# Performance work log

Measured on AMD Instinct MI355X. Metric: run time of the kernel, lower is better.

The kernel has to match this reference:

```python
import jax, jax.numpy as jnp
import numpy as np

N, E, F_IN, H, D, HID, G = 50000, 800000, 64, 4, 32, 128, 1024
NEG_SLOPE = 0.2


def setup_inputs():
    key = jax.random.key(0)
    ks = jax.random.split(key, 32)
    inp = {
        "x": jax.random.normal(ks[0], (N, F_IN), dtype=jnp.float32),
        "edge_index": jax.random.randint(ks[1], (2, E), 0, N, dtype=jnp.int64),
        "batch": jnp.sort(jax.random.randint(ks[2], (N,), 0, G, dtype=jnp.int64)),
    }
    dims = [F_IN, HID, HID]
    i = 3
    for l, din in enumerate(dims):
        s = 1.0 / np.sqrt(din)
        inp[f"Wl{l}"] = jax.random.normal(ks[i], (din, H * D), dtype=jnp.float32) * s; i += 1
        inp[f"bl{l}"] = jnp.zeros((H * D,), dtype=jnp.float32)
        inp[f"Wr{l}"] = jax.random.normal(ks[i], (din, H * D), dtype=jnp.float32) * s; i += 1
        inp[f"br{l}"] = jnp.zeros((H * D,), dtype=jnp.float32)
        inp[f"att{l}"] = jax.random.normal(ks[i], (H, D), dtype=jnp.float32) * (1.0 / np.sqrt(D)); i += 1
        inp[f"b{l}"] = jnp.zeros((H * D,), dtype=jnp.float32)
    inp["Wh"] = jax.random.normal(ks[i], (HID, 1), dtype=jnp.float32) * (1.0 / np.sqrt(HID))
    inp["bh"] = jnp.zeros((1,), dtype=jnp.float32)
    return inp


def gatv2_layer(x, src, dst, Wl, bl, Wr, br, att, b):
    # GATv2Conv (eval mode, no dropout): e_ij = att . leaky_relu(Wl x_j + Wr x_i)
    xl = (x @ Wl + bl).reshape(-1, H, D)   # source transform
    xr = (x @ Wr + br).reshape(-1, H, D)   # target transform
    m = xl[src] + xr[dst]                  # [E,H,D]
    e = jnp.where(m >= 0, m, NEG_SLOPE * m)
    score = jnp.einsum("ehd,hd->eh", e, att)          # [E,H]
    smax = jax.ops.segment_max(score, dst, num_segments=N)  # [N,H]
    expv = jnp.exp(score - smax[dst])
    denom = jax.ops.segment_sum(expv, dst, num_segments=N)
    alpha = expv / denom[dst]                          # softmax over in-edges of dst
    agg = jax.ops.segment_sum(alpha[:, :, None] * xl[src], dst, num_segments=N)
    return agg.reshape(-1, H * D) + b


def reference(x, edge_index, batch, Wl0, bl0, Wr0, br0, att0, b0,
              Wl1, bl1, Wr1, br1, att1, b1,
              Wl2, bl2, Wr2, br2, att2, b2, Wh, bh):
    src, dst = edge_index[0], edge_index[1]
    params = [(Wl0, bl0, Wr0, br0, att0, b0),
              (Wl1, bl1, Wr1, br1, att1, b1),
              (Wl2, bl2, Wr2, br2, att2, b2)]
    h = x
    for p in params:
        h = gatv2_layer(h, src, dst, *p)
        h = jax.nn.elu(h)  # dropout inactive in eval
    # global mean pool over graphs
    sums = jax.ops.segment_sum(h, batch, num_segments=G)
    cnt = jax.ops.segment_sum(jnp.ones((h.shape[0],), h.dtype), batch, num_segments=G)
    pooled = sums / jnp.maximum(cnt, 1.0)[:, None]
    return pooled @ Wh + bh
```

## Files before the change

### kernel.cpp

```cpp
#include <hip/hip_runtime.h>
#include <math.h>

#define N_NODES 50000
#define N_EDGES 800000
#define HD 128
#define GG 1024
#define NEG_SLOPE 0.2f
#define SCAN_B 1024
#define NB ((N_NODES + SCAN_B - 1) / SCAN_B)
#define NXCONV (N_NODES * 64)

typedef __attribute__((ext_vector_type(8))) short bf16x8;
typedef __attribute__((ext_vector_type(4))) float f32x4;

__device__ __forceinline__ unsigned short f2bf(float v) {
    unsigned u = __float_as_uint(v);
    u += 0x7fff + ((u >> 16) & 1);
    return (unsigned short)(u >> 16);
}
__device__ __forceinline__ float bf2f(unsigned short s) {
    return __uint_as_float((unsigned)s << 16);
}

__global__ void convert_all(const float* __restrict__ x,
                            unsigned short* __restrict__ Xh, unsigned short* __restrict__ Xl,
                            const float* __restrict__ W0l, const float* __restrict__ W0r,
                            const float* __restrict__ W1l, const float* __restrict__ W1r,
                            const float* __restrict__ W2l, const float* __restrict__ W2r,
                            unsigned short* __restrict__ Wth, unsigned short* __restrict__ Wtl,
                            int* __restrict__ deg)
{
    const int i = blockIdx.x * 256 + threadIdx.x;
    if (i < N_NODES) deg[i] = 0;
    if (i < NXCONV) {
        const float v = x[i];
        const unsigned short hi = f2bf(v);
        Xh[i] = hi;
        Xl[i] = f2bf(v - bf2f(hi));
        return;
    }
    const int t = i - NXCONV;
    const float* Wl; const float* Wr;
    int c, k, o;
    if (t < 16384) {
        c = t >> 6; k = t & 63; o = t;
        Wl = W0l; Wr = W0r;
    } else if (t < 49152) {
        const int b = t - 16384; c = b >> 7; k = b & 127; o = 32768 + b;
        Wl = W1l; Wr = W1r;
    } else if (t < 81920) {
        const int b = t - 49152; c = b >> 7; k = b & 127; o = 65536 + b;
        Wl = W2l; Wr = W2r;
    } else return;
    const float v = (c < 128) ? Wl[(size_t)k * 128 + c] : Wr[(size_t)k * 128 + (c - 128)];
    const unsigned short hi = f2bf(v);
    Wth[o] = hi;
    Wtl[o] = f2bf(v - bf2f(hi));
}

__global__ void prep_graph(const int* __restrict__ dst, int* __restrict__ deg,
                           const int* __restrict__ batch, int* __restrict__ gptr)
{
    const int e = blockIdx.x * 256 + threadIdx.x;
    if (e < N_EDGES) atomicAdd(&deg[dst[e]], 1);
    if (e > N_NODES) return;
    if (e == 0) {
        for (int g = 0; g <= batch[0]; g++) gptr[g] = 0;
    } else if (e == N_NODES) {
        for (int g = batch[N_NODES - 1] + 1; g <= GG; g++) gptr[g] = N_NODES;
    } else {
        const int b0 = batch[e - 1], b1 = batch[e];
        for (int g = b0 + 1; g <= b1; g++) gptr[g] = e;
    }
}

template<int K>
__launch_bounds__(256, 3)
__global__ void gemm_lds(const unsigned short* __restrict__ Xh, const unsigned short* __restrict__ Xl,
                         const unsigned short* __restrict__ Wth, const unsigned short* __restrict__ Wtl,
                         const float* __restrict__ bl, const float* __restrict__ br,
                         float* __restrict__ Cl, float* __restrict__ Cr, int n)
{
    constexpr int NCH = K / 32;
    constexpr int STR = K + 8;
    __shared__ unsigned short AsH[64 * STR], AsL[64 * STR];
    const int tid  = threadIdx.x;
    const int wave = tid >> 6;
    const int lane = tid & 63;
    const int quad = lane >> 4;
    const int l15  = lane & 15;
    const int cg   = blockIdx.x & 1;
    const int rt   = blockIdx.x >> 1;
    const int row0 = rt * 64;
    const int colid = cg * 4 + wave;
    const int cb32  = colid * 32;

    bf16x8 Bh[NCH][2], Bo[NCH][2];
    #pragma unroll
    for (int ch = 0; ch < NCH; ch++)
        #pragma unroll
        for (int nt = 0; nt < 2; nt++) {
            const size_t wo = (size_t)(cb32 + nt * 16 + l15) * K + ch * 32 + quad * 8;
            Bh[ch][nt] = *(const bf16x8*)(Wth + wo);
            Bo[ch][nt] = *(const bf16x8*)(Wtl + wo);
        }

    {
        constexpr int THR = K / 8;
        constexpr int RPP = 256 / THR;
        const int sr = tid / THR, seg = tid % THR;
        #pragma unroll
        for (int ps = 0; ps < 64 / RPP; ps++) {
            const int r = ps * RPP + sr;
            int gr = row0 + r;
            gr = (gr < n) ? gr : (n - 1);
            const size_t go = (size_t)gr * K + seg * 8;
            *(uint4*)&AsH[r * STR + seg * 8] = *(const uint4*)(Xh + go);
            *(uint4*)&AsL[r * STR + seg * 8] = *(const uint4*)(Xl + go);
        }
    }
    __syncthreads();

    f32x4 acc[4][2];
    #pragma unroll
    for (int mt = 0; mt < 4; mt++) {
        acc[mt][0] = (f32x4){0.f, 0.f, 0.f, 0.f};
        acc[mt][1] = (f32x4){0.f, 0.f, 0.f, 0.f};
    }
    #pragma unroll
    for (int ch = 0; ch < NCH; ch++) {
        bf16x8 ah[4], al[4];
        #pragma unroll
        for (int mt = 0; mt < 4; mt++) {
            ah[mt] = *(const bf16x8*)&AsH[(mt * 16 + l15) * STR + ch * 32 + quad * 8];
            al[mt] = *(const bf16x8*)&AsL[(mt * 16 + l15) * STR + ch * 32 + quad * 8];
        }
        #pragma unroll
        for (int nt = 0; nt < 2; nt++)
            #pragma unroll
            for (int mt = 0; mt < 4; mt++) {
                acc[mt][nt] = __builtin_amdgcn_mfma_f32_16x16x32_bf16(ah[mt], Bh[ch][nt], acc[mt][nt], 0, 0, 0);
                acc[mt][nt] = __builtin_amdgcn_mfma_f32_16x16x32_bf16(ah[mt], Bo[ch][nt], acc[mt][nt], 0, 0, 0);
                acc[mt][nt] = __builtin_amdgcn_mfma_f32_16x16x32_bf16(al[mt], Bh[ch][nt], acc[mt][nt], 0, 0, 0);
            }
    }

    const int cb = cb32 & 127;
    const float* bias = (colid < 4) ? bl : br;
    float* C = (colid < 4) ? Cl : Cr;
    const float bv0 = bias[cb + l15];
    const float bv1 = bias[cb + 16 + l15];
    #pragma unroll
    for (int nt = 0; nt < 2; nt++) {
        const float bv = nt ? bv1 : bv0;
        #pragma unroll
        for (int mt = 0; mt < 4; mt++)
            #pragma unroll
            for (int r = 0; r < 4; r++) {
                const int row = row0 + mt * 16 + quad * 4 + r;
                if (row < n)
                    C[(size_t)row * 128 + cb + nt * 16 + l15] = acc[mt][nt][r] + bv;
            }
    }
}

__launch_bounds__(SCAN_B)
__global__ void scan_block(const int* __restrict__ deg, int* __restrict__ rowptr,
                           int* __restrict__ btot)
{
    __shared__ int s[SCAN_B];
    const int tid = threadIdx.x;
    const int i = blockIdx.x * SCAN_B + tid;
    int v = (i < N_NODES) ? deg[i] : 0;
    s[tid] = v;
    __syncthreads();
    for (int off = 1; off < SCAN_B; off <<= 1) {
        int t = (tid >= off) ? s[tid - off] : 0;
        __syncthreads();
        s[tid] += t;
        __syncthreads();
    }
    if (i < N_NODES) rowptr[i] = s[tid] - v;
    if (tid == SCAN_B - 1) btot[blockIdx.x] = s[SCAN_B - 1];
}

__launch_bounds__(256)
__global__ void scan_add(const int* __restrict__ btot, int* __restrict__ rowptr,
                         int* __restrict__ cursor)
{
    __shared__ int sb[NB + 1];
    const int tid = threadIdx.x;
    if (tid < 64) {
        const int v = (tid < NB) ? btot[tid] : 0;
        int incl = v;
        #pragma unroll
        for (int off = 1; off < 64; off <<= 1) {
            const int t = __shfl_up(incl, off);
            if (tid >= off) incl += t;
        }
        if (tid < NB) sb[tid] = incl - v;
        if (tid == NB - 1) sb[NB] = incl;
    }
    __syncthreads();
    const int i = blockIdx.x * 256 + tid;
    if (i < N_NODES) {
        const int r = rowptr[i] + sb[i >> 10];
        rowptr[i] = r;
        cursor[i] = r;
    }
    if (i == N_NODES) rowptr[N_NODES] = sb[NB];
}

__global__ void scatter_csr(const int* __restrict__ src, const int* __restrict__ dst,
                            int* __restrict__ cursor, int* __restrict__ csr_src)
{
    int e = blockIdx.x * 256 + threadIdx.x;
    if (e >= N_EDGES) return;
    int pos = atomicAdd(&cursor[dst[e]], 1);
    csr_src[pos] = src[e];
}

template<int LAST>
__launch_bounds__(256)
__global__ void node_attn(const float* __restrict__ xl, const float* __restrict__ xr,
                          const int* __restrict__ rowptr, const int* __restrict__ csr_src,
                          const float* __restrict__ att, const float* __restrict__ bvec,
                          unsigned short* __restrict__ Hh, unsigned short* __restrict__ Hl,
                          const float* __restrict__ Wh, float* __restrict__ pernode)
{
    const int node = (blockIdx.x * 256 + threadIdx.x) >> 6;
    const int lane = threadIdx.x & 63;
    if (node >= N_NODES) return;
    const int grp = lane >> 4;
    const int li  = lane & 15;

    const size_t nb = (size_t)node * HD + li * 8;
    const float4 xr0 = *(const float4*)(xr + nb);
    const float4 xr1 = *(const float4*)(xr + nb + 4);
    const float4 aw0 = *(const float4*)(att + li * 8);
    const float4 aw1 = *(const float4*)(att + li * 8 + 4);
    const int beg = rowptr[node];
    const int end = rowptr[node + 1];

    float m = -1e30f, l = 0.f;
    float4 a0 = make_float4(0.f, 0.f, 0.f, 0.f);
    float4 a1 = make_float4(0.f, 0.f, 0.f, 0.f);

    int e0 = beg + grp;
    int s0 = (e0 < end) ? csr_src[e0] : 0;
    float4 v0 = *(const float4*)(xl + (size_t)s0 * HD + li * 8);
    float4 v1 = *(const float4*)(xl + (size_t)s0 * HD + li * 8 + 4);

    for (int base = beg; base < end; base += 4) {
        const bool valid = (base + grp) < end;
        float4 n0 = v0, n1 = v1;
        if (base + 4 < end) {
            const int e2 = base + 4 + grp;
            const int s2 = (e2 < end) ? csr_src[e2] : 0;
            n0 = *(const float4*)(xl + (size_t)s2 * HD + li * 8);
            n1 = *(const float4*)(xl + (size_t)s2 * HD + li * 8 + 4);
        }
        float t, pa, pb;
        t = v0.x + xr0.x; t = fmaxf(t, NEG_SLOPE * t); pa = t * aw0.x;
        t = v0.y + xr0.y; t = fmaxf(t, NEG_SLOPE * t); pb = t * aw0.y;
        t = v0.z + xr0.z; t = fmaxf(t, NEG_SLOPE * t); pa = fmaf(t, aw0.z, pa);
        t = v0.w + xr0.w; t = fmaxf(t, NEG_SLOPE * t); pb = fmaf(t, aw0.w, pb);
        t = v1.x + xr1.x; t = fmaxf(t, NEG_SLOPE * t); pa = fmaf(t, aw1.x, pa);
        t = v1.y + xr1.y; t = fmaxf(t, NEG_SLOPE * t); pb = fmaf(t, aw1.y, pb);
        t = v1.z + xr1.z; t = fmaxf(t, NEG_SLOPE * t); pa = fmaf(t, aw1.z, pa);
        t = v1.w + xr1.w; t = fmaxf(t, NEG_SLOPE * t); pb = fmaf(t, aw1.w, pb);
        float p = pa + pb;
        p += __shfl_xor(p, 1);
        p += __shfl_xor(p, 2);

        const float mn = valid ? fmaxf(m, p) : m;
        const float w  = valid ? __expf(p - mn) : 0.f;
        const float sc = __expf(m - mn);
        l = fmaf(l, sc, w);
        a0.x = fmaf(a0.x, sc, w * v0.x);
        a0.y = fmaf(a0.y, sc, w * v0.y);
        a0.z = fmaf(a0.z, sc, w * v0.z);
        a0.w = fmaf(a0.w, sc, w * v0.w);
        a1.x = fmaf(a1.x, sc, w * v1.x);
        a1.y = fmaf(a1.y, sc, w * v1.y);
        a1.z = fmaf(a1.z, sc, w * v1.z);
        a1.w = fmaf(a1.w, sc, w * v1.w);
        m = mn;
        v0 = n0; v1 = n1;
    }

    #pragma unroll
    for (int off = 16; off < 64; off <<= 1) {
        const float mo = __shfl_xor(m, off);
        const float lo = __shfl_xor(l, off);
        float4 b0, b1;
        b0.x = __shfl_xor(a0.x, off); b0.y = __shfl_xor(a0.y, off);
        b0.z = __shfl_xor(a0.z, off); b0.w = __shfl_xor(a0.w, off);
        b1.x = __shfl_xor(a1.x, off); b1.y = __shfl_xor(a1.y, off);
        b1.z = __shfl_xor(a1.z, off); b1.w = __shfl_xor(a1.w, off);
        const float mm = fmaxf(m, mo);
        const float e1 = __expf(m - mm);
        const float e2 = __expf(mo - mm);
        l = l * e1 + lo * e2;
        a0.x = a0.x * e1 + b0.x * e2;
        a0.y = a0.y * e1 + b0.y * e2;
        a0.z = a0.z * e1 + b0.z * e2;
        a0.w = a0.w * e1 + b0.w * e2;
        a1.x = a1.x * e1 + b1.x * e2;
        a1.y = a1.y * e1 + b1.y * e2;
        a1.z = a1.z * e1 + b1.z * e2;
        a1.w = a1.w * e1 + b1.w * e2;
        m = mm;
    }

    if (grp == 0) {
        const float inv = (l > 0.f) ? 1.f / l : 0.f;
        const float4 bb0 = *(const float4*)(bvec + li * 8);
        const float4 bb1 = *(const float4*)(bvec + li * 8 + 4);
        float o[8];
        o[0] = fmaf(a0.x, inv, bb0.x);
        o[1] = fmaf(a0.y, inv, bb0.y);
        o[2] = fmaf(a0.z, inv, bb0.z);
        o[3] = fmaf(a0.w, inv, bb0.w);
        o[4] = fmaf(a1.x, inv, bb1.x);
        o[5] = fmaf(a1.y, inv, bb1.y);
        o[6] = fmaf(a1.z, inv, bb1.z);
        o[7] = fmaf(a1.w, inv, bb1.w);
        #pragma unroll
        for (int j = 0; j < 8; j++)
            o[j] = (o[j] > 0.f) ? o[j] : expm1f(o[j]);
        if (LAST) {
            const float4 w0 = *(const float4*)(Wh + li * 8);
            const float4 w1 = *(const float4*)(Wh + li * 8 + 4);
            float da = o[0] * w0.x + o[2] * w0.z;
            float db = o[1] * w0.y + o[3] * w0.w;
            da = fmaf(o[4], w1.x, da); db = fmaf(o[5], w1.y, db);
            da = fmaf(o[6], w1.z, da); db = fmaf(o[7], w1.w, db);
            float d = da + db;
            d += __shfl_xor(d, 1);
            d += __shfl_xor(d, 2);
            d += __shfl_xor(d, 4);
            d += __shfl_xor(d, 8);
            if (li == 0) pernode[node] = d;
        } else {
            bf16x8 hv, lv;
            #pragma unroll
            for (int j = 0; j < 8; j++) {
                unsigned short h = f2bf(o[j]);
                hv[j] = (short)h;
                lv[j] = (short)f2bf(o[j] - bf2f(h));
            }
            *(bf16x8*)(Hh + nb) = hv;
            *(bf16x8*)(Hl + nb) = lv;
        }
    }
}

__launch_bounds__(256)
__global__ void finish_head(const float* __restrict__ pernode, const int* __restrict__ gptr,
                            const float* __restrict__ bh, float* __restrict__ out)
{
    const int g = (blockIdx.x * 256 + threadIdx.x) >> 6;
    const int lane = threadIdx.x & 63;
    if (g >= GG) return;
    const int b0 = gptr[g], b1 = gptr[g + 1];
    float s = 0.f;
    for (int i = b0 + lane; i < b1; i += 64) s += pernode[i];
    s += __shfl_xor(s, 1);
    s += __shfl_xor(s, 2);
    s += __shfl_xor(s, 4);
    s += __shfl_xor(s, 8);
    s += __shfl_xor(s, 16);
    s += __shfl_xor(s, 32);
    if (lane == 0) out[g] = s / fmaxf((float)(b1 - b0), 1.f) + bh[0];
}

extern "C" void kernel_launch(void* const* d_in, const int* in_sizes, int n_in,
                              void* d_out, int out_size, void* d_ws, size_t ws_size,
                              hipStream_t stream)
{
    const float* x     = (const float*)d_in[0];
    const int*   edge  = (const int*)d_in[1];
    const int*   batch = (const int*)d_in[2];
    const int*   src   = edge;
    const int*   dst   = edge + N_EDGES;
    const float* Wh    = (const float*)d_in[21];
    const float* bh    = (const float*)d_in[22];
    float* out = (float*)d_out;

    const size_t N128 = (size_t)N_NODES * HD;
    float* buf_xl = (float*)d_ws;
    float* buf_xr = buf_xl + N128;
    unsigned short* Xh  = (unsigned short*)(buf_xr + N128);
    unsigned short* Xl_ = Xh + N128;
    unsigned short* Wth = Xl_ + N128;
    unsigned short* Wtl = Wth + 3 * 256 * 128;
    int* deg       = (int*)(Wtl + 3 * 256 * 128);
    float* pernode = (float*)(deg + N_NODES);
    int* rowptr  = (int*)(pernode + N_NODES);
    int* cursor  = rowptr + N_NODES + 1;
    int* csr_src = cursor + N_NODES;
    int* btot    = csr_src + N_EDGES;
    int* gptr    = btot + NB;

    convert_all<<<(NXCONV + 81920 + 255) / 256, 256, 0, stream>>>(
        x, Xh, Xl_,
        (const float*)d_in[3], (const float*)d_in[5],
        (const float*)d_in[9], (const float*)d_in[11],
        (const float*)d_in[15], (const float*)d_in[17],
        Wth, Wtl, deg);
    prep_graph<<<(N_EDGES + 255) / 256, 256, 0, stream>>>(dst, deg, batch, gptr);
    scan_block<<<NB, SCAN_B, 0, stream>>>(deg, rowptr, btot);
    scan_add<<<(N_NODES + 256) / 256, 256, 0, stream>>>(btot, rowptr, cursor);
    scatter_csr<<<(N_EDGES + 255) / 256, 256, 0, stream>>>(src, dst, cursor, csr_src);

    const int gemm_grid = ((N_NODES + 63) / 64) * 2;
    const int attn_grid = (N_NODES + 3) / 4;

    for (int l = 0; l < 3; l++) {
        const float* bl  = (const float*)d_in[4 + 6 * l];
        const float* br  = (const float*)d_in[6 + 6 * l];
        const float* att = (const float*)d_in[7 + 6 * l];
        const float* bb  = (const float*)d_in[8 + 6 * l];

        if (l == 0)
            gemm_lds<64><<<gemm_grid, 256, 0, stream>>>(Xh, Xl_, Wth, Wtl,
                                                        bl, br, buf_xl, buf_xr, N_NODES);
        else
            gemm_lds<128><<<gemm_grid, 256, 0, stream>>>(Xh, Xl_,
                                                         Wth + l * 256 * 128, Wtl + l * 256 * 128,
                                                         bl, br, buf_xl, buf_xr, N_NODES);
        if (l < 2)
            node_attn<0><<<attn_grid, 256, 0, stream>>>(buf_xl, buf_xr, rowptr, csr_src,
                                                        att, bb, Xh, Xl_,
                                                        nullptr, nullptr);
        else
            node_attn<1><<<attn_grid, 256, 0, stream>>>(buf_xl, buf_xr, rowptr, csr_src,
                                                        att, bb, nullptr, nullptr,
                                                        Wh, pernode);
    }

    finish_head<<<GG / 4, 256, 0, stream>>>(pernode, gptr, bh, out);
}
```

Baseline: 478.5 us.

## Merge prep kernels, single-block scan, persistent GEMM grid, packed f32x2 attention math

Fuses conversion and graph-prep into one launch, with deg zeroed by a memset. The two-kernel scan is replaced by a single 1024-thread block that scans 49 elements per thread. The GEMM becomes a persistent grid-stride loop over row tiles with a fixed grid of 512, with B fragments loaded once per block and the occupancy hint dropped. The attention inner loop uses 2-wide float vectors, aiming for packed FP32 instructions. Together these cut launch count and per-block weight reloads, at the cost of a serial single-block scan and possibly lower GEMM occupancy.

```diff
diff --git a/kernel.cpp b/kernel.cpp
--- a/kernel.cpp
+++ b/kernel.cpp
@@ -6,12 +6,12 @@
 #define HD 128
 #define GG 1024
 #define NEG_SLOPE 0.2f
-#define SCAN_B 1024
-#define NB ((N_NODES + SCAN_B - 1) / SCAN_B)
 #define NXCONV (N_NODES * 64)
+#define NWCONV 81920
 
 typedef __attribute__((ext_vector_type(8))) short bf16x8;
 typedef __attribute__((ext_vector_type(4))) float f32x4;
+typedef __attribute__((ext_vector_type(2))) float f32x2;
 
 __device__ __forceinline__ unsigned short f2bf(float v) {
     unsigned u = __float_as_uint(v);
@@ -22,16 +22,16 @@
     return __uint_as_float((unsigned)s << 16);
 }
 
-__global__ void convert_all(const float* __restrict__ x,
-                            unsigned short* __restrict__ Xh, unsigned short* __restrict__ Xl,
-                            const float* __restrict__ W0l, const float* __restrict__ W0r,
-                            const float* __restrict__ W1l, const float* __restrict__ W1r,
-                            const float* __restrict__ W2l, const float* __restrict__ W2r,
-                            unsigned short* __restrict__ Wth, unsigned short* __restrict__ Wtl,
-                            int* __restrict__ deg)
+__global__ void convert_prep(const float* __restrict__ x,
+                             unsigned short* __restrict__ Xh, unsigned short* __restrict__ Xl,
+                             const float* __restrict__ W0l, const float* __restrict__ W0r,
+                             const float* __restrict__ W1l, const float* __restrict__ W1r,
+                             const float* __restrict__ W2l, const float* __restrict__ W2r,
+                             unsigned short* __restrict__ Wth, unsigned short* __restrict__ Wtl,
+                             const int* __restrict__ dst, int* __restrict__ deg,
+                             const int* __restrict__ batch, int* __restrict__ gptr)
 {
     const int i = blockIdx.x * 256 + threadIdx.x;
-    if (i < N_NODES) deg[i] = 0;
     if (i < NXCONV) {
         const float v = x[i];
         const unsigned short hi = f2bf(v);
@@ -39,29 +39,27 @@
         Xl[i] = f2bf(v - bf2f(hi));
         return;
     }
-    const int t = i - NXCONV;
-    const float* Wl; const float* Wr;
-    int c, k, o;
-    if (t < 16384) {
-        c = t >> 6; k = t & 63; o = t;
-        Wl = W0l; Wr = W0r;
-    } else if (t < 49152) {
-        const int b = t - 16384; c = b >> 7; k = b & 127; o = 32768 + b;
-        Wl = W1l; Wr = W1r;
-    } else if (t < 81920) {
-        const int b = t - 49152; c = b >> 7; k = b & 127; o = 65536 + b;
-        Wl = W2l; Wr = W2r;
-    } else return;
-    const float v = (c < 128) ? Wl[(size_t)k * 128 + c] : Wr[(size_t)k * 128 + (c - 128)];
-    const unsigned short hi = f2bf(v);
-    Wth[o] = hi;
-    Wtl[o] = f2bf(v - bf2f(hi));
-}
-
-__global__ void prep_graph(const int* __restrict__ dst, int* __restrict__ deg,
-                           const int* __restrict__ batch, int* __restrict__ gptr)
-{
-    const int e = blockIdx.x * 256 + threadIdx.x;
+    if (i < NXCONV + NWCONV) {
+        const int t = i - NXCONV;
+        const float* Wl; const float* Wr;
+        int c, k, o;
+        if (t < 16384) {
+            c = t >> 6; k = t & 63; o = t;
+            Wl = W0l; Wr = W0r;
+        } else if (t < 49152) {
+            const int b = t - 16384; c = b >> 7; k = b & 127; o = 32768 + b;
+            Wl = W1l; Wr = W1r;
+        } else {
+            const int b = t - 49152; c = b >> 7; k = b & 127; o = 65536 + b;
+            Wl = W2l; Wr = W2r;
+        }
+        const float v = (c < 128) ? Wl[(size_t)k * 128 + c] : Wr[(size_t)k * 128 + (c - 128)];
+        const unsigned short hi = f2bf(v);
+        Wth[o] = hi;
+        Wtl[o] = f2bf(v - bf2f(hi));
+        return;
+    }
+    const int e = i - NXCONV - NWCONV;
     if (e < N_EDGES) atomicAdd(&deg[dst[e]], 1);
     if (e > N_NODES) return;
     if (e == 0) {
@@ -74,8 +72,52 @@
     }
 }
 
+#define SPT 49
+__launch_bounds__(1024)
+__global__ void scan_all(const int* __restrict__ deg, int* __restrict__ rowptr,
+                         int* __restrict__ cursor)
+{
+    __shared__ int ps[1024];
+    const int tid = threadIdx.x;
+    const int base = tid * SPT;
+    int s = 0;
+    #pragma unroll
+    for (int j = 0; j < SPT; j++) {
+        const int idx = base + j;
+        s += (idx < N_NODES) ? deg[idx] : 0;
+    }
+    ps[tid] = s;
+    __syncthreads();
+    for (int off = 1; off < 1024; off <<= 1) {
+        const int t = (tid >= off) ? ps[tid - off] : 0;
+        __syncthreads();
+        ps[tid] += t;
+        __syncthreads();
+    }
+    int run = ps[tid] - s;
+    #pragma unroll
+    for (int j = 0; j < SPT; j++) {
+        const int idx = base + j;
+        if (idx < N_NODES) {
+            rowptr[idx] = run;
+            cursor[idx] = run;
+            run += deg[idx];
+        }
+    }
+    if (tid == 1023) rowptr[N_NODES] = ps[1023];
+}
+
+__global__ void scatter_csr(const int* __restrict__ src, const int* __restrict__ dst,
+                            int* __restrict__ cursor, int* __restrict__ csr_src)
+{
+    int e = blockIdx.x * 256 + threadIdx.x;
+    if (e >= N_EDGES) return;
+    int pos = atomicAdd(&cursor[dst[e]], 1);
+    csr_src[pos] = src[e];
+}
+
 template<int K>
-__launch_bounds__(256, 3)
+__launch_bounds__(256)
 __global__ void gemm_lds(const unsigned short* __restrict__ Xh, const unsigned short* __restrict__ Xl,
                          const unsigned short* __restrict__ Wth, const unsigned short* __restrict__ Wtl,
                          const float* __restrict__ bl, const float* __restrict__ br,
@@ -83,6 +125,7 @@
 {
     constexpr int NCH = K / 32;
     constexpr int STR = K + 8;
+    constexpr int RT  = (N_NODES + 63) / 64;
     __shared__ unsigned short AsH[64 * STR], AsL[64 * STR];
     const int tid  = threadIdx.x;
     const int wave = tid >> 6;
@@ -90,8 +133,8 @@
     const int quad = lane >> 4;
     const int l15  = lane & 15;
     const int cg   = blockIdx.x & 1;
-    const int rt   = blockIdx.x >> 1;
-    const int row0 = rt * 64;
+    const int rs   = blockIdx.x >> 1;
+    const int NS   = gridDim.x >> 1;
     const int colid = cg * 4 + wave;
     const int cb32  = colid * 32;
 
@@ -104,120 +147,69 @@
             Bh[ch][nt] = *(const bf16x8*)(Wth + wo);
             Bo[ch][nt] = *(const bf16x8*)(Wtl + wo);
         }
-
-    {
-        constexpr int THR = K / 8;
-        constexpr int RPP = 256 / THR;
-        const int sr = tid / THR, seg = tid % THR;
-        #pragma unroll
-        for (int ps = 0; ps < 64 / RPP; ps++) {
-            const int r = ps * RPP + sr;
-            int gr = row0 + r;
-            gr = (gr < n) ? gr : (n - 1);
-            const size_t go = (size_t)gr * K + seg * 8;
-            *(uint4*)&AsH[r * STR + seg * 8] = *(const uint4*)(Xh + go);
-            *(uint4*)&AsL[r * STR + seg * 8] = *(const uint4*)(Xl + go);
-        }
-    }
-    __syncthreads();
-
-    f32x4 acc[4][2];
-    #pragma unroll
-    for (int mt = 0; mt < 4; mt++) {
-        acc[mt][0] = (f32x4){0.f, 0.f, 0.f, 0.f};
-        acc[mt][1] = (f32x4){0.f, 0.f, 0.f, 0.f};
-    }
-    #pragma unroll
-    for (int ch = 0; ch < NCH; ch++) {
-        bf16x8 ah[4], al[4];
-        #pragma unroll
-        for (int mt = 0; mt < 4; mt++) {
-            ah[mt] = *(const bf16x8*)&AsH[(mt * 16 + l15) * STR + ch * 32 + quad * 8];
-            al[mt] = *(const bf16x8*)&AsL[(mt * 16 + l15) * STR + ch * 32 + quad * 8];
-        }
-        #pragma unroll
-        for (int nt = 0; nt < 2; nt++)
-            #pragma unroll
-            for (int mt = 0; mt < 4; mt++) {
-                acc[mt][nt] = __builtin_amdgcn_mfma_f32_16x16x32_bf16(ah[mt], Bh[ch][nt], acc[mt][nt], 0, 0, 0);
-                acc[mt][nt] = __builtin_amdgcn_mfma_f32_16x16x32_bf16(ah[mt], Bo[ch][nt], acc[mt][nt], 0, 0, 0);
-                acc[mt][nt] = __builtin_amdgcn_mfma_f32_16x16x32_bf16(al[mt], Bh[ch][nt], acc[mt][nt], 0, 0, 0);
-            }
-    }
 
     const int cb = cb32 & 127;
     const float* bias = (colid < 4) ? bl : br;
     float* C = (colid < 4) ? Cl : Cr;
     const float bv0 = bias[cb + l15];
     const float bv1 = bias[cb + 16 + l15];
-    #pragma unroll
-    for (int nt = 0; nt < 2; nt++) {
-        const float bv = nt ? bv1 : bv0;
-        #pragma unroll
-        for (int mt = 0; mt < 4; mt++)
+
+    for (int rt = rs; rt < RT; rt += NS) {
+        const int row0 = rt * 64;
+        {
+            constexpr int THR = K / 8;
+            constexpr int RPP = 256 / THR;
+            const int sr = tid / THR, seg = tid % THR;
             #pragma unroll
-            for (int r = 0; r < 4; r++) {
-                const int row = row0 + mt * 16 + quad * 4 + r;
-                if (row < n)
-                    C[(size_t)row * 128 + cb + nt * 16 + l15] = acc[mt][nt][r] + bv;
+            for (int ps = 0; ps < 64 / RPP; ps++) {
+                const int r = ps * RPP + sr;
+                int gr = row0 + r;
+                gr = (gr < n) ? gr : (n - 1);
+                const size_t go = (size_t)gr * K + seg * 8;
+                *(uint4*)&AsH[r * STR + seg * 8] = *(const uint4*)(Xh + go);
+                *(uint4*)&AsL[r * STR + seg * 8] = *(const uint4*)(Xl + go);
             }
-    }
-}
-
-__launch_bounds__(SCAN_B)
-__global__ void scan_block(const int* __restrict__ deg, int* __restrict__ rowptr,
-                           int* __restrict__ btot)
-{
-    __shared__ int s[SCAN_B];
-    const int tid = threadIdx.x;
-    const int i = blockIdx.x * SCAN_B + tid;
-    int v = (i < N_NODES) ? deg[i] : 0;
-    s[tid] = v;
-    __syncthreads();
-    for (int off = 1; off < SCAN_B; off <<= 1) {
-        int t = (tid >= off) ? s[tid - off] : 0;
+        }
         __syncthreads();
-        s[tid] += t;
+
+        f32x4 acc[4][2];
+        #pragma unroll
+        for (int mt = 0; mt < 4; mt++) {
+            acc[mt][0] = (f32x4){0.f, 0.f, 0.f, 0.f};
+            acc[mt][1] = (f32x4){0.f, 0.f, 0.f, 0.f};
+        }
+        #pragma unroll
+        for (int ch = 0; ch < NCH; ch++) {
+            bf16x8 ah[4], al[4];
+            #pragma unroll
+            for (int mt = 0; mt < 4; mt++) {
+                ah[mt] = *(const bf16x8*)&AsH[(mt * 16 + l15) * STR + ch * 32 + quad * 8];
+                al[mt] = *(const bf16x8*)&AsL[(mt * 16 + l15) * STR + ch * 32 + quad * 8];
+            }
+            #pragma unroll
+            for (int nt = 0; nt < 2; nt++)
+                #pragma unroll
+                for (int mt = 0; mt < 4; mt++) {
+                    acc[mt][nt] = __builtin_amdgcn_mfma_f32_16x16x32_bf16(ah[mt], Bh[ch][nt], acc[mt][nt], 0, 0, 0);
+                    acc[mt][nt] = __builtin_amdgcn_mfma_f32_16x16x32_bf16(ah[mt], Bo[ch][nt], acc[mt][nt], 0, 0, 0);
+                    acc[mt][nt] = __builtin_amdgcn_mfma_f32_16x16x32_bf16(al[mt], Bh[ch][nt], acc[mt][nt], 0, 0, 0);
+                }
+        }
+
+        #pragma unroll
+        for (int nt = 0; nt < 2; nt++) {
+            const float bv = nt ? bv1 : bv0;
+            #pragma unroll
+            for (int mt = 0; mt < 4; mt++)
+                #pragma unroll
+                for (int r = 0; r < 4; r++) {
+                    const int row = row0 + mt * 16 + quad * 4 + r;
+                    if (row < n)
+                        C[(size_t)row * 128 + cb + nt * 16 + l15] = acc[mt][nt][r] + bv;
+                }
+        }
         __syncthreads();
     }
-    if (i < N_NODES) rowptr[i] = s[tid] - v;
-    if (tid == SCAN_B - 1) btot[blockIdx.x] = s[SCAN_B - 1];
-}
-
-__launch_bounds__(256)
-__global__ void scan_add(const int* __restrict__ btot, int* __restrict__ rowptr,
-                         int* __restrict__ cursor)
-{
-    __shared__ int sb[NB + 1];
-    const int tid = threadIdx.x;
-    if (tid < 64) {
-        const int v = (tid < NB) ? btot[tid] : 0;
-        int incl = v;
-        #pragma unroll
-        for (int off = 1; off < 64; off <<= 1) {
-            const int t = __shfl_up(incl, off);
-            if (tid >= off) incl += t;
-        }
-        if (tid < NB) sb[tid] = incl - v;
-        if (tid == NB - 1) sb[NB] = incl;
-    }
-    __syncthreads();
-    const int i = blockIdx.x * 256 + tid;
-    if (i < N_NODES) {
-        const int r = rowptr[i] + sb[i >> 10];
-        rowptr[i] = r;
-        cursor[i] = r;
-    }
-    if (i == N_NODES) rowptr[N_NODES] = sb[NB];
-}
-
-__global__ void scatter_csr(const int* __restrict__ src, const int* __restrict__ dst,
-                            int* __restrict__ cursor, int* __restrict__ csr_src)
-{
-    int e = blockIdx.x * 256 + threadIdx.x;
-    if (e >= N_EDGES) return;
-    int pos = atomicAdd(&cursor[dst[e]], 1);
-    csr_src[pos] = src[e];
 }
 
 template<int LAST>
@@ -235,41 +227,61 @@
     const int li  = lane & 15;
 
     const size_t nb = (size_t)node * HD + li * 8;
-    const float4 xr0 = *(const float4*)(xr + nb);
-    const float4 xr1 = *(const float4*)(xr + nb + 4);
-    const float4 aw0 = *(const float4*)(att + li * 8);
-    const float4 aw1 = *(const float4*)(att + li * 8 + 4);
+    f32x2 xrp[4], awp[4];
+    {
+        const float4 a = *(const float4*)(xr + nb);
+        const float4 b = *(const float4*)(xr + nb + 4);
+        xrp[0] = (f32x2){a.x, a.y}; xrp[1] = (f32x2){a.z, a.w};
+        xrp[2] = (f32x2){b.x, b.y}; xrp[3] = (f32x2){b.z, b.w};
+        const float4 c = *(const float4*)(att + li * 8);
+        const float4 d = *(const float4*)(att + li * 8 + 4);
+        awp[0] = (f32x2){c.x, c.y}; awp[1] = (f32x2){c.z, c.w};
+        awp[2] = (f32x2){d.x, d.y}; awp[3] = (f32x2){d.z, d.w};
+    }
+    const f32x2 nsl = (f32x2){NEG_SLOPE, NEG_SLOPE};
     const int beg = rowptr[node];
     const int end = rowptr[node + 1];
 
     float m = -1e30f, l = 0.f;
-    float4 a0 = make_float4(0.f, 0.f, 0.f, 0.f);
-    float4 a1 = make_float4(0.f, 0.f, 0.f, 0.f);
-
-    int e0 = beg + grp;
-    int s0 = (e0 < end) ? csr_src[e0] : 0;
-    float4 v0 = *(const float4*)(xl + (size_t)s0 * HD + li * 8);
-    float4 v1 = *(const float4*)(xl + (size_t)s0 * HD + li * 8 + 4);
+    f32x2 accp[4];
+    #pragma unroll
+    for (int j = 0; j < 4; j++) accp[j] = (f32x2){0.f, 0.f};
+
+    f32x2 vp[4];
+    {
+        const int e0 = beg + grp;
+        const int s0 = (e0 < end) ? csr_src[e0] : 0;
+        const float4 a = *(const float4*)(xl + (size_t)s0 * HD + li * 8);
+        const float4 b = *(const float4*)(xl + (size_t)s0 * HD + li * 8 + 4);
+        vp[0] = (f32x2){a.x, a.y}; vp[1] = (f32x2){a.z, a.w};
+        vp[2] = (f32x2){b.x, b.y}; vp[3] = (f32x2){b.z, b.w};
+    }
 
     for (int base = beg; base < end; base += 4) {
         const bool valid = (base + grp) < end;
-        float4 n0 = v0, n1 = v1;
+        f32x2 np[4];
+        #pragma unroll
+        for (int j = 0; j < 4; j++) np[j] = vp[j];
         if (base + 4 < end) {
             const int e2 = base + 4 + grp;
             const int s2 = (e2 < end) ? csr_src[e2] : 0;
-            n0 = *(const float4*)(xl + (size_t)s2 * HD + li * 8);
-            n1 = *(const float4*)(xl + (size_t)s2 * HD + li * 8 + 4);
-        }
-        float t, pa, pb;
-        t = v0.x + xr0.x; t = fmaxf(t, NEG_SLOPE * t); pa = t * aw0.x;
-        t = v0.y + xr0.y; t = fmaxf(t, NEG_SLOPE * t); pb = t * aw0.y;
-        t = v0.z + xr0.z; t = fmaxf(t, NEG_SLOPE * t); pa = fmaf(t, aw0.z, pa);
-        t = v0.w + xr0.w; t = fmaxf(t, NEG_SLOPE * t); pb = fmaf(t, aw0.w, pb);
-        t = v1.x + xr1.x; t = fmaxf(t, NEG_SLOPE * t); pa = fmaf(t, aw1.x, pa);
-        t = v1.y + xr1.y; t = fmaxf(t, NEG_SLOPE * t); pb = fmaf(t, aw1.y, pb);
-        t = v1.z + xr1.z; t = fmaxf(t, NEG_SLOPE * t); pa = fmaf(t, aw1.z, pa);
-        t = v1.w + xr1.w; t = fmaxf(t, NEG_SLOPE * t); pb = fmaf(t, aw1.w, pb);
-        float p = pa + pb;
+            const float4 a = *(const float4*)(xl + (size_t)s2 * HD + li * 8);
+            const float4 b = *(const float4*)(xl + (size_t)s2 * HD + li * 8 + 4);
+            np[0] = (f32x2){a.x, a.y}; np[1] = (f32x2){a.z, a.w};
+            np[2] = (f32x2){b.x, b.y}; np[3] = (f32x2){b.z, b.w};
+        }
+        f32x2 pd0 = (f32x2){0.f, 0.f}, pd1 = (f32x2){0.f, 0.f};
+        #pragma unroll
+        for (int j = 0; j < 4; j++) {
+            f32x2 t = vp[j] + xrp[j];
+            const f32x2 u = t * nsl;
+            t[0] = fmaxf(t[0], u[0]);
+            t[1] = fmaxf(t[1], u[1]);
+            if (j & 1) pd1 = t * awp[j] + pd1;
+            else       pd0 = t * awp[j] + pd0;
+        }
+        const f32x2 pds = pd0 + pd1;
+        float p = pds[0] + pds[1];
         p += __shfl_xor(p, 1);
         p += __shfl_xor(p, 2);
 
@@ -277,39 +289,35 @@
         const float w  = valid ? __expf(p - mn) : 0.f;
         const float sc = __expf(m - mn);
         l = fmaf(l, sc, w);
-        a0.x = fmaf(a0.x, sc, w * v0.x);
-        a0.y = fmaf(a0.y, sc, w * v0.y);
-        a0.z = fmaf(a0.z, sc, w * v0.z);
-        a0.w = fmaf(a0.w, sc, w * v0.w);
-        a1.x = fmaf(a1.x, sc, w * v1.x);
-        a1.y = fmaf(a1.y, sc, w * v1.y);
-        a1.z = fmaf(a1.z, sc, w * v1.z);
-        a1.w = fmaf(a1.w, sc, w * v1.w);
+        const f32x2 w2  = (f32x2){w, w};
+        const f32x2 sc2 = (f32x2){sc, sc};
+        #pragma unroll
+        for (int j = 0; j < 4; j++) {
+            accp[j] = accp[j] * sc2 + w2 * vp[j];
+            vp[j] = np[j];
+        }
         m = mn;
-        v0 = n0; v1 = n1;
     }
 
     #pragma unroll
     for (int off = 16; off < 64; off <<= 1) {
         const float mo = __shfl_xor(m, off);
         const float lo = __shfl_xor(l, off);
-        float4 b0, b1;
-        b0.x = __shfl_xor(a0.x, off); b0.y = __shfl_xor(a0.y, off);
-        b0.z = __shfl_xor(a0.z, off); b0.w = __shfl_xor(a0.w, off);
-        b1.x = __shfl_xor(a1.x, off); b1.y = __shfl_xor(a1.y, off);
-        b1.z = __shfl_xor(a1.z, off); b1.w = __shfl_xor(a1.w, off);
+        f32x2 bo[4];
+        #pragma unroll
+        for (int j = 0; j < 4; j++) {
+            bo[j][0] = __shfl_xor(accp[j][0], off);
+            bo[j][1] = __shfl_xor(accp[j][1], off);
+        }
         const float mm = fmaxf(m, mo);
         const float e1 = __expf(m - mm);
         const float e2 = __expf(mo - mm);
         l = l * e1 + lo * e2;
-        a0.x = a0.x * e1 + b0.x * e2;
-        a0.y = a0.y * e1 + b0.y * e2;
-        a0.z = a0.z * e1 + b0.z * e2;
-        a0.w = a0.w * e1 + b0.w * e2;
-        a1.x = a1.x * e1 + b1.x * e2;
-        a1.y = a1.y * e1 + b1.y * e2;
-        a1.z = a1.z * e1 + b1.z * e2;
-        a1.w = a1.w * e1 + b1.w * e2;
+        const f32x2 e1p = (f32x2){e1, e1};
+        const f32x2 e2p = (f32x2){e2, e2};
+        #pragma unroll
+        for (int j = 0; j < 4; j++)
+            accp[j] = accp[j] * e1p + bo[j] * e2p;
         m = mm;
     }
 
@@ -318,14 +326,14 @@
         const float4 bb0 = *(const float4*)(bvec + li * 8);
         const float4 bb1 = *(const float4*)(bvec + li * 8 + 4);
         float o[8];
-        o[0] = fmaf(a0.x, inv, bb0.x);
-        o[1] = fmaf(a0.y, inv, bb0.y);
-        o[2] = fmaf(a0.z, inv, bb0.z);
-        o[3] = fmaf(a0.w, inv, bb0.w);
-        o[4] = fmaf(a1.x, inv, bb1.x);
-        o[5] = fmaf(a1.y, inv, bb1.y);
-        o[6] = fmaf(a1.z, inv, bb1.z);
-        o[7] = fmaf(a1.w, inv, bb1.w);
+        o[0] = fmaf(accp[0][0], inv, bb0.x);
+        o[1] = fmaf(accp[0][1], inv, bb0.y);
+        o[2] = fmaf(accp[1][0], inv, bb0.z);
+        o[3] = fmaf(accp[1][1], inv, bb0.w);
+        o[4] = fmaf(accp[2][0], inv, bb1.x);
+        o[5] = fmaf(accp[2][1], inv, bb1.y);
+        o[6] = fmaf(accp[3][0], inv, bb1.z);
+        o[7] = fmaf(accp[3][1], inv, bb1.w);
         #pragma unroll
         for (int j = 0; j < 8; j++)
             o[j] = (o[j] > 0.f) ? o[j] : expm1f(o[j]);
@@ -400,21 +408,19 @@
     int* rowptr  = (int*)(pernode + N_NODES);
     int* cursor  = rowptr + N_NODES + 1;
     int* csr_src = cursor + N_NODES;
-    int* btot    = csr_src + N_EDGES;
-    int* gptr    = btot + NB;
-
-    convert_all<<<(NXCONV + 81920 + 255) / 256, 256, 0, stream>>>(
+    int* gptr    = csr_src + N_EDGES;
+
+    hipMemsetAsync(deg, 0, (size_t)N_NODES * sizeof(int), stream);
+    convert_prep<<<(NXCONV + NWCONV + N_EDGES + 255) / 256, 256, 0, stream>>>(
         x, Xh, Xl_,
         (const float*)d_in[3], (const float*)d_in[5],
         (const float*)d_in[9], (const float*)d_in[11],
         (const float*)d_in[15], (const float*)d_in[17],
-        Wth, Wtl, deg);
-    prep_graph<<<(N_EDGES + 255) / 256, 256, 0, stream>>>(dst, deg, batch, gptr);
-    scan_block<<<NB, SCAN_B, 0, stream>>>(deg, rowptr, btot);
-    scan_add<<<(N_NODES + 256) / 256, 256, 0, stream>>>(btot, rowptr, cursor);
+        Wth, Wtl, dst, deg, batch, gptr);
+    scan_all<<<1, 1024, 0, stream>>>(deg, rowptr, cursor);
     scatter_csr<<<(N_EDGES + 255) / 256, 256, 0, stream>>>(src, dst, cursor, csr_src);
 
-    const int gemm_grid = ((N_NODES + 63) / 64) * 2;
+    const int gemm_grid = 512;
     const int attn_grid = (N_NODES + 3) / 4;
 
     for (int l = 0; l < 3; l++) {
```

After: 541.8 us. +13.2%, slower.
